# Performance work log

Measured on AMD Instinct MI355X. Metric: run time of the kernel, lower is better.

Reference implementation:

```python
import jax, jax.numpy as jnp
import numpy as np

Q_DEFAULT = 8
XI_MAX = 0.4          # center frequency of the highest-frequency wavelet (cycles/sample)
BW_RATIO = 0.8        # bandwidth-to-center-frequency ratio
LOG_EPS = 1e-6


def _make_filters(T, Q):
    """Morlet-style analytic filter bank in the Fourier domain (all static numpy)."""
    J = int(np.floor(np.log2(T / 2)))
    freqs = np.fft.fftfreq(T).astype(np.float32)          # [T], in [-0.5, 0.5)
    # first-order wavelets: J*Q filters, geometrically spaced, quality factor Q
    n1 = J * Q
    xi1 = (XI_MAX * 2.0 ** (-np.arange(n1) / Q)).astype(np.float32)
    sig1 = (BW_RATIO * xi1 / Q).astype(np.float32)
    psi1 = np.exp(-(freqs[None, :] - xi1[:, None]) ** 2 / (2.0 * sig1[:, None] ** 2)).astype(np.float32)  # [n1, T]
    # second-order wavelets: Q2 = 1, one per octave
    xi2 = (XI_MAX * 2.0 ** (-np.arange(J))).astype(np.float32)
    sig2 = (BW_RATIO * xi2).astype(np.float32)
    psi2 = np.exp(-(freqs[None, :] - xi2[:, None]) ** 2 / (2.0 * sig2[:, None] ** 2)).astype(np.float32)  # [J, T]
    # low-pass (phi): Gaussian at scale 2^J
    sigma_phi = np.float32(BW_RATIO * XI_MAX * 2.0 ** (-J))
    phi = np.exp(-(freqs ** 2) / (2.0 * sigma_phi ** 2)).astype(np.float32)  # [T]
    # valid second-order paths: xi2 strictly below xi1 (frequency-decreasing cascade)
    pair_j1, pair_k = [], []
    for k in range(J):
        for j1 in range(n1):
            if xi2[k] < xi1[j1]:
                pair_j1.append(j1)
                pair_k.append(k)
    return psi1, psi2, phi, np.asarray(pair_j1, np.int32), np.asarray(pair_k, np.int32)


def _scatter(x_flat, psi1, psi2, phi, pair_j1, pair_k):
    """x_flat: [N, T] real. Returns S: [N, 1 + n1 + n_pairs, T]."""
    xh = jnp.fft.fft(x_flat)                                   # [N, T] complex
    S0 = jnp.fft.ifft(xh * phi).real[:, None, :]               # order 0 (dropped later)
    U1 = jnp.abs(jnp.fft.ifft(xh[:, None, :] * psi1[None]))    # [N, n1, T]
    U1h = jnp.fft.fft(U1)
    S1 = jnp.fft.ifft(U1h * phi).real                          # [N, n1, T]
    U2 = jnp.abs(jnp.fft.ifft(U1h[:, pair_j1, :] * psi2[pair_k][None]))  # [N, P, T]
    S2 = jnp.fft.ifft(jnp.fft.fft(U2) * phi).real              # [N, P, T]
    return jnp.concatenate([S0, S1, S2], axis=1)


def setup_inputs() -> dict:
    key = jax.random.key(0)
    x = jax.random.normal(key, (8, 2048, 6), dtype=jnp.float32)
    return {"x": x}


def reference(x):
    B, T, C = x.shape
    psi1, psi2, phi, pj, pk = _make_filters(T, Q_DEFAULT)
    psi1, psi2, phi = jnp.asarray(psi1), jnp.asarray(psi2), jnp.asarray(phi)
    # vectorize the original per-channel Python loop: fold channels into batch
    xf = jnp.transpose(x, (0, 2, 1)).reshape(B * C, T)          # [B*C, T]
    S = _scatter(xf, psi1, psi2, phi, pj, pk)                   # [B*C, n_coef+1, T]
    out = jnp.mean(jnp.log(S[:, 1:, :] + LOG_EPS), axis=-1)     # drop order-0, log, time-mean
    return out.reshape(B, C, -1).transpose(0, 2, 1)             # [B, n_coef, C]
```

## Files before the change

kernel.cpp:

```cpp
#include <hip/hip_runtime.h>

#define NTH 256
#define U1H_STRIDE 21504

#define PHI1 0.29504296f
#define PHI2 0.0075683594f
#define GCUT 18.0f

__device__ __forceinline__ int swz(int i) { return i ^ (((i >> 4) & 3) * 5); }

__device__ __forceinline__ float2 cmul(float2 a, float2 b) {
  return make_float2(a.x * b.x - a.y * b.y, a.x * b.y + a.y * b.x);
}

template <int W>
__device__ __forceinline__ float wsum(float v) {
#pragma unroll
  for (int off = 1; off < W; off <<= 1) v += __shfl_xor(v, off, 64);
  return v;
}

__device__ __forceinline__ float2 shflx2(float2 v, int mask) {
  return make_float2(__shfl_xor(v.x, mask, 64), __shfl_xor(v.y, mask, 64));
}

template <int M, int LANES, bool INV>
__device__ __forceinline__ void rdif(float2* x, int l) {
  constexpr int R = M / LANES;
#pragma unroll
  for (int half = R / 2; half >= 1; half >>= 1) {
    const int s = half * LANES;
    const float a0 = (INV ? 3.14159265358979f : -3.14159265358979f) / (float)s;
#pragma unroll
    for (int r = 0; r < R; ++r) {
      if ((r & half) == 0) {
        const float2 a = x[r], b = x[r + half];
        const int j = (r & (half - 1)) * LANES + l;
        float2 w; __sincosf(a0 * (float)j, &w.y, &w.x);
        x[r] = make_float2(a.x + b.x, a.y + b.y);
        x[r + half] = cmul(make_float2(a.x - b.x, a.y - b.y), w);
      }
    }
  }
#pragma unroll
  for (int s = LANES / 2; s >= 1; s >>= 1) {
    const float a0 = (INV ? 3.14159265358979f : -3.14159265358979f) / (float)s;
    float2 w; __sincosf(a0 * (float)(l & (s - 1)), &w.y, &w.x);
    const bool hi = (l & s) != 0;
#pragma unroll
    for (int r = 0; r < R; ++r) {
      const float2 y = shflx2(x[r], s);
      const float2 sum = make_float2(x[r].x + y.x, x[r].y + y.y);
      const float2 dif = cmul(make_float2(y.x - x[r].x, y.y - x[r].y), w);
      x[r] = hi ? dif : sum;
    }
  }
}

template <int M, int LANES, bool INV>
__device__ __forceinline__ void rdit(float2* x, int l) {
  constexpr int R = M / LANES;
#pragma unroll
  for (int s = 1; s <= LANES / 2; s <<= 1) {
    const float a0 = (INV ? 3.14159265358979f : -3.14159265358979f) / (float)s;
    float2 w; __sincosf(a0 * (float)(l & (s - 1)), &w.y, &w.x);
    const bool hi = (l & s) != 0;
#pragma unroll
    for (int r = 0; r < R; ++r) {
      const float2 y = shflx2(x[r], s);
      const float2 wb = cmul(w, hi ? x[r] : y);
      x[r] = hi ? make_float2(y.x - wb.x, y.y - wb.y)
                : make_float2(x[r].x + wb.x, x[r].y + wb.y);
    }
  }
#pragma unroll
  for (int half = 1; half <= R / 2; half <<= 1) {
    const int s = half * LANES;
    const float a0 = (INV ? 3.14159265358979f : -3.14159265358979f) / (float)s;
#pragma unroll
    for (int r = 0; r < R; ++r) {
      if ((r & half) == 0) {
        const int j = (r & (half - 1)) * LANES + l;
        float2 w; __sincosf(a0 * (float)j, &w.y, &w.x);
        const float2 bw = cmul(x[r + half], w);
        const float2 a = x[r];
        x[r] = make_float2(a.x + bw.x, a.y + bw.y);
        x[r + half] = make_float2(a.x - bw.x, a.y - bw.y);
      }
    }
  }
}

template <bool INV>
__device__ __forceinline__ void dif4(float2* A, int j, int ls, float astep) {
  const int s = 1 << ls;
  const int e = j & (s - 1);
  const int base = ((j >> ls) << (ls + 2)) | e;
  float2 w1;
  __sincosf(astep * (float)e, &w1.y, &w1.x);
  if (INV) w1.y = -w1.y;
  const float2 w2 = cmul(w1, w1);
  const float2 w3 = cmul(w2, w1);
  const float2 a0 = A[swz(base)];
  const float2 a1 = A[swz(base + s)];
  const float2 a2 = A[swz(base + 2 * s)];
  const float2 a3 = A[swz(base + 3 * s)];
  const float t0x = a0.x + a2.x, t0y = a0.y + a2.y;
  const float t1x = a0.x - a2.x, t1y = a0.y - a2.y;
  const float t2x = a1.x + a3.x, t2y = a1.y + a3.y;
  const float bdx = a1.x - a3.x, bdy = a1.y - a3.y;
  const float sgn = INV ? -1.0f : 1.0f;
  const float t3x = sgn * bdy, t3y = -sgn * bdx;
  A[swz(base)]         = make_float2(t0x + t2x, t0y + t2y);
  A[swz(base + s)]     = cmul(make_float2(t1x + t3x, t1y + t3y), w1);
  A[swz(base + 2 * s)] = cmul(make_float2(t0x - t2x, t0y - t2y), w2);
  A[swz(base + 3 * s)] = cmul(make_float2(t1x - t3x, t1y - t3y), w3);
}

__device__ __forceinline__ void r2pair(float2* A, int g) {
  const float2 a = A[swz(2 * g)];
  const float2 b = A[swz(2 * g + 1)];
  A[swz(2 * g)]     = make_float2(a.x + b.x, a.y + b.y);
  A[swz(2 * g + 1)] = make_float2(a.x - b.x, a.y - b.y);
}

__device__ __forceinline__ int prev2048(int i) {
  return ((i >> 9) & 3) | (((i >> 7) & 3) << 2) | (((i >> 5) & 3) << 4) |
         (((i >> 3) & 3) << 6) | (((i >> 1) & 3) << 8) | ((i & 1) << 10);
}

__global__ __launch_bounds__(NTH) void kA(const float* __restrict__ x,
                                          float2* __restrict__ xh) {
  __shared__ float2 A[2048];
  const int n = blockIdx.x, b = n / 6, c = n % 6;
  const float* xp = x + (size_t)b * (2048 * 6) + c;
#pragma unroll
  for (int i = 0; i < 8; ++i) {
    const int t = (int)threadIdx.x + NTH * i;
    A[swz(t)] = make_float2(xp[t * 6], 0.0f);
  }
  const int tid = (int)threadIdx.x;
#pragma unroll
  for (int ls = 9; ls >= 1; ls -= 2) {
    const float astep = -1.5707963267948966f / (float)(1 << ls);
    __syncthreads();
#pragma unroll
    for (int i = 0; i < 2; ++i) dif4<false>(A, tid + NTH * i, ls, astep);
  }
  __syncthreads();
#pragma unroll
  for (int i = 0; i < 4; ++i) r2pair(A, tid + NTH * i);
  __syncthreads();
#pragma unroll
  for (int i = 0; i < 8; ++i) {
    const int t = (int)threadIdx.x + NTH * i;
    xh[(size_t)n * 2048 + prev2048(t)] = A[swz(t)];
  }
}

__device__ __forceinline__ int u1h_off(int j1) {
  const int o = j1 >> 3;
  if (o == 0) return j1 * 1024;
  if (o == 1) return 8192 + (j1 - 8) * 512;
  if (o == 2) return 12288 + (j1 - 16) * 256;
  return 14336 + (j1 - 24) * 128;
}
__device__ __forceinline__ float* o1p(float* out, int b, int c, int j1) {
  return out + ((size_t)b * 440 + j1) * 6 + c;
}
__device__ __forceinline__ float* o2p(float* out, int b, int c, int j1, int k) {
  return out + ((size_t)b * 440 + 80 + 4 * k * (k - 1) + j1) * 6 + c;
}
__device__ __forceinline__ float xi2f(int k) { return 0.4f * exp2f(-(float)k); }

template <int M1, int LANES>
__device__ __forceinline__ void parentR(const float2* __restrict__ src,
                                        float2* __restrict__ Vg,
                                        float* __restrict__ outp,
                                        int j1, int lane) {
  constexpr int R = M1 / LANES;
  constexpr int F = 2048 / M1;
  const int l = lane & (LANES - 1);
  const int gb = lane - l;
  const float xi = 0.4f * exp2f(-0.125f * (float)j1);
  const float sig = 0.1f * xi;
  const float i2s = 1.0f / (2.0f * sig * sig);
  float2 x[R];
#pragma unroll
  for (int r = 0; r < R; ++r) {
    const int m = r * LANES + l;
    float2 acc = make_float2(0.0f, 0.0f);
#pragma unroll
    for (int q = 0; q < F; ++q) {
      const int f = m + q * M1;
      const float fr = (float)(f < 1024 ? f : f - 2048) * (1.0f / 2048.0f);
      const float d = fr - xi;
      const float dd = d * d * i2s;
      if (dd < GCUT) {
        const float g = __expf(-dd);
        const float2 v = src[f];
        acc.x += v.x * g; acc.y += v.y * g;
      }
    }
    x[r] = acc;
  }
  rdif<M1, LANES, true>(x, l);
#pragma unroll
  for (int r = 0; r < R; ++r)
    x[r] = make_float2(sqrtf(x[r].x * x[r].x + x[r].y * x[r].y) * (1.0f / 2048.0f), 0.0f);
  rdit<M1, LANES, false>(x, l);
#pragma unroll
  for (int r = 0; r < R; ++r) Vg[r * LANES + l] = x[r];
  const float invM = 1.0f / (float)M1;
  const float c0 = __shfl(x[0].x, gb, 64) * invM;
  const float2 U1 = make_float2(__shfl(x[0].x, gb + 1, 64), __shfl(x[0].y, gb + 1, 64));
  const float2 U2 = make_float2(__shfl(x[0].x, gb + 2, 64), __shfl(x[0].y, gb + 2, 64));
  const float k1 = PHI1 * 2.0f * invM, k2 = PHI2 * 2.0f * invM;
  float part = 0.0f;
#pragma unroll
  for (int r = 0; r < R; ++r) {
    const int t = r * LANES + l;
    float sv, cv;
    __sincosf((6.283185307179586f / (float)M1) * (float)t, &sv, &cv);
    float acc = c0 + k1 * (U1.x * cv - U1.y * sv);
    const float c2 = cv * cv - sv * sv, s2 = 2.0f * sv * cv;
    acc += k2 * (U2.x * c2 - U2.y * s2);
    part += __logf(acc + 1e-6f);
  }
  part = wsum<LANES>(part);
  if (l == 0) *outp = part * invM;
}

__global__ __launch_bounds__(NTH, 4) void kB(const float2* __restrict__ xh,
                                             float2* __restrict__ U1h,
                                             float* __restrict__ out) {
  const int ci = (int)blockIdx.x / 48;
  const int n  = (int)blockIdx.x % 48;
  const int b = n / 6, c = n % 6;
  const float2* src = xh + (size_t)n * 2048;
  float2* Vb = U1h + (size_t)n * U1H_STRIDE;
  const int tid = (int)threadIdx.x;
  const int wid = tid >> 6, lane = tid & 63;
  const int h = lane >> 5;
  const int slot = 2 * wid + h;

  if (ci < 2) {
    const int j1 = 4 * ci + wid;
    parentR<1024, 64>(src, Vb + u1h_off(j1), o1p(out, b, c, j1), j1, lane);
  } else if (ci < 4) {
    const int j1 = 8 + 4 * (ci - 2) + wid;
    parentR<512, 64>(src, Vb + u1h_off(j1), o1p(out, b, c, j1), j1, lane);
  } else if (ci < 6) {
    const int j1 = 16 + 4 * (ci - 4) + wid;
    parentR<256, 64>(src, Vb + u1h_off(j1), o1p(out, b, c, j1), j1, lane);
  } else {
    const int j1 = 24 + 8 * (ci - 6) + slot;
    parentR<128, 32>(src, Vb + u1h_off(j1), o1p(out, b, c, j1), j1, lane);
  }
}

template <int M2, int LANES>
__device__ __forceinline__ void descR(const float2* __restrict__ Vg,
                                      float* __restrict__ outp,
                                      int M1, int F, float xi, int lane) {
  constexpr int R = M2 / LANES;
  constexpr int LM = (M2 == 1024) ? 10 : (M2 == 512) ? 9 : (M2 == 256) ? 8 : 7;
  const int l = lane & (LANES - 1);
  const float sg = 0.8f * xi;
  const float i2s = 1.0f / (2.0f * sg * sg);
  float2 x[R];
#pragma unroll
  for (int r = 0; r < R; ++r) {
    const int m = r * LANES + l;
    float2 acc = make_float2(0.0f, 0.0f);
    for (int q = 0; q < F; ++q) {
      const int f = m + q * M2;
      const float fr = (float)(f < (M1 >> 1) ? f : f - M1) * (1.0f / 2048.0f);
      const float d = fr - xi;
      const float dd = d * d * i2s;
      if (dd < GCUT) {
        const float g = __expf(-dd);
        const float2 vv = Vg[f];
        acc.x += vv.x * g; acc.y += vv.y * g;
      }
    }
    x[r] = acc;
  }
  rdif<M2, LANES, true>(x, l);
  const float invM1f = 1.0f / (float)M1;
  float b0 = 0, b1r = 0, b1i = 0, b2r = 0, b2i = 0;
#pragma unroll
  for (int r = 0; r < R; ++r) {
    const float u = sqrtf(x[r].x * x[r].x + x[r].y * x[r].y) * invM1f;
    const int e = r * LANES + l;
    const int t = (int)(__brev((unsigned)e) >> (32 - LM));
    float sv, cv;
    __sincosf((6.283185307179586f / (float)M2) * (float)t, &sv, &cv);
    b0 += u;
    b1r += u * cv; b1i -= u * sv;
    const float c2 = cv * cv - sv * sv, s2 = 2.0f * sv * cv;
    b2r += u * c2; b2i -= u * s2;
  }
  b0 = wsum<LANES>(b0);
  b1r = wsum<LANES>(b1r); b1i = wsum<LANES>(b1i);
  b2r = wsum<LANES>(b2r); b2i = wsum<LANES>(b2i);
  const float k1 = 2.0f * PHI1, k2 = 2.0f * PHI2;
  const float invM2 = 1.0f / (float)M2;
  float part = 0.0f;
#pragma unroll
  for (int r = 0; r < R; ++r) {
    const int e = r * LANES + l;
    const int t = (int)(__brev((unsigned)e) >> (32 - LM));
    float sv, cv;
    __sincosf((6.283185307179586f / (float)M2) * (float)t, &sv, &cv);
    float acc = b0 + k1 * (b1r * cv - b1i * sv);
    const float c2 = cv * cv - sv * sv, s2 = 2.0f * sv * cv;
    acc += k2 * (b2r * c2 - b2i * s2);
    part += __logf(acc * invM2 + 1e-6f);
  }
  part = wsum<LANES>(part);
  if (l == 0) *outp = part * invM2;
}

__global__ __launch_bounds__(NTH, 4) void kC(const float2* __restrict__ U1h,
                                             float* __restrict__ out) {
  const int ci = (int)blockIdx.x / 48;
  const int n  = (int)blockIdx.x % 48;
  const int b = n / 6, c = n % 6;
  const float2* Vb = U1h + (size_t)n * U1H_STRIDE;
  const int tid = (int)threadIdx.x;
  const int wid = tid >> 6, lane = tid & 63;
  const int h = lane >> 5;
  const int slot = 2 * wid + h;

  if (ci < 2) {
    const int j1 = 4 * ci + wid;
    descR<1024, 64>(Vb + u1h_off(j1), o2p(out, b, c, j1, 1), 1024, 1, xi2f(1), lane);
  } else if (ci < 6) {
    const int j1 = 4 * (ci - 2) + wid;
    const int M1 = (j1 < 8) ? 1024 : 512;
    descR<512, 64>(Vb + u1h_off(j1), o2p(out, b, c, j1, 2), M1, M1 / 512, xi2f(2), lane);
  } else if (ci < 8) {
    const int j1 = 4 * (ci - 6) + wid;
    descR<512, 64>(Vb + u1h_off(j1), o2p(out, b, c, j1, 3), 1024, 2, xi2f(3), lane);
  } else if (ci < 12) {
    const int j1 = 8 + 4 * (ci - 8) + wid;
    const int M1 = (j1 < 16) ? 512 : 256;
    descR<256, 64>(Vb + u1h_off(j1), o2p(out, b, c, j1, 3), M1, M1 / 256, xi2f(3), lane);
  } else if (ci < 14) {
    const int j1 = 4 * (ci - 12) + wid;
    descR<256, 64>(Vb + u1h_off(j1), o2p(out, b, c, j1, 4), 1024, 4, xi2f(4), lane);
  } else if (ci < 17) {
    const int j1 = 8 + 8 * (ci - 14) + slot;
    const int o = j1 >> 3;
    const int M1 = (o < 3) ? (1024 >> o) : 128;
    descR<128, 32>(Vb + u1h_off(j1), o2p(out, b, c, j1, 4), M1, M1 / 128, xi2f(4), lane);
  } else {
    int g = ci - 17;
    int k = 5;
    while (g >= k) { g -= k; ++k; }
    const int j1 = 8 * g + slot;
    const int M1 = (g < 3) ? (1024 >> g) : 128;
    descR<128, 32>(Vb + u1h_off(j1), o2p(out, b, c, j1, k), M1, M1 / 128, xi2f(k), lane);
  }
}

extern "C" void kernel_launch(void* const* d_in, const int* in_sizes, int n_in,
                              void* d_out, int out_size, void* d_ws, size_t ws_size,
                              hipStream_t stream) {
  (void)in_sizes; (void)n_in; (void)out_size; (void)ws_size;
  const float* x = (const float*)d_in[0];
  float* out = (float*)d_out;
  float2* U1h = (float2*)d_ws;
  float2* xh = (float2*)((char*)d_ws + (size_t)48 * U1H_STRIDE * sizeof(float2));
  kA<<<dim3(48), dim3(NTH), 0, stream>>>(x, xh);
  kB<<<dim3(13 * 48), dim3(NTH), 0, stream>>>(xh, U1h, out);
  kC<<<dim3(52 * 48), dim3(NTH), 0, stream>>>(U1h, out);
}
```

Before: 99.50 us.

## Fuse first- and second-order stages into one kernel with recomputed parents in LDS

Merges kernels kB and kC into a single kernel kU. Each wave or half-wave recomputes its first-order parent U1h from xh, then runs its second-order descendant on it directly in shared memory. This removes the global U1h round trip and one kernel launch. The register/shuffle radix-2 FFTs are replaced by radix-4 shared-memory FFTs. The trade-off is that each parent FFT is now redone for every descendant, and the extra shared memory may lower occupancy.

```diff
diff --git a/kernel.cpp b/kernel.cpp
--- a/kernel.cpp
+++ b/kernel.cpp
@@ -1,7 +1,6 @@
 #include <hip/hip_runtime.h>
 
 #define NTH 256
-#define U1H_STRIDE 21504
 
 #define PHI1 0.29504296f
 #define PHI2 0.0075683594f
@@ -20,75 +19,21 @@
   return v;
 }
 
-__device__ __forceinline__ float2 shflx2(float2 v, int mask) {
-  return make_float2(__shfl_xor(v.x, mask, 64), __shfl_xor(v.y, mask, 64));
-}
-
-template <int M, int LANES, bool INV>
-__device__ __forceinline__ void rdif(float2* x, int l) {
-  constexpr int R = M / LANES;
-#pragma unroll
-  for (int half = R / 2; half >= 1; half >>= 1) {
-    const int s = half * LANES;
-    const float a0 = (INV ? 3.14159265358979f : -3.14159265358979f) / (float)s;
-#pragma unroll
-    for (int r = 0; r < R; ++r) {
-      if ((r & half) == 0) {
-        const float2 a = x[r], b = x[r + half];
-        const int j = (r & (half - 1)) * LANES + l;
-        float2 w; __sincosf(a0 * (float)j, &w.y, &w.x);
-        x[r] = make_float2(a.x + b.x, a.y + b.y);
-        x[r + half] = cmul(make_float2(a.x - b.x, a.y - b.y), w);
-      }
-    }
-  }
-#pragma unroll
-  for (int s = LANES / 2; s >= 1; s >>= 1) {
-    const float a0 = (INV ? 3.14159265358979f : -3.14159265358979f) / (float)s;
-    float2 w; __sincosf(a0 * (float)(l & (s - 1)), &w.y, &w.x);
-    const bool hi = (l & s) != 0;
-#pragma unroll
-    for (int r = 0; r < R; ++r) {
-      const float2 y = shflx2(x[r], s);
-      const float2 sum = make_float2(x[r].x + y.x, x[r].y + y.y);
-      const float2 dif = cmul(make_float2(y.x - x[r].x, y.y - x[r].y), w);
-      x[r] = hi ? dif : sum;
-    }
-  }
-}
-
-template <int M, int LANES, bool INV>
-__device__ __forceinline__ void rdit(float2* x, int l) {
-  constexpr int R = M / LANES;
-#pragma unroll
-  for (int s = 1; s <= LANES / 2; s <<= 1) {
-    const float a0 = (INV ? 3.14159265358979f : -3.14159265358979f) / (float)s;
-    float2 w; __sincosf(a0 * (float)(l & (s - 1)), &w.y, &w.x);
-    const bool hi = (l & s) != 0;
-#pragma unroll
-    for (int r = 0; r < R; ++r) {
-      const float2 y = shflx2(x[r], s);
-      const float2 wb = cmul(w, hi ? x[r] : y);
-      x[r] = hi ? make_float2(y.x - wb.x, y.y - wb.y)
-                : make_float2(x[r].x + wb.x, x[r].y + wb.y);
-    }
-  }
-#pragma unroll
-  for (int half = 1; half <= R / 2; half <<= 1) {
-    const int s = half * LANES;
-    const float a0 = (INV ? 3.14159265358979f : -3.14159265358979f) / (float)s;
-#pragma unroll
-    for (int r = 0; r < R; ++r) {
-      if ((r & half) == 0) {
-        const int j = (r & (half - 1)) * LANES + l;
-        float2 w; __sincosf(a0 * (float)j, &w.y, &w.x);
-        const float2 bw = cmul(x[r + half], w);
-        const float2 a = x[r];
-        x[r] = make_float2(a.x + bw.x, a.y + bw.y);
-        x[r + half] = make_float2(a.x - bw.x, a.y - bw.y);
-      }
-    }
-  }
+template <int M>
+__device__ __forceinline__ int prevM(int i) {
+  if (M == 128)
+    return ((i >> 5) & 3) | (((i >> 3) & 3) << 2) | (((i >> 1) & 3) << 4) | ((i & 1) << 6);
+  else if (M == 256)
+    return ((i & 3) << 6) | (((i >> 2) & 3) << 4) | (((i >> 4) & 3) << 2) | ((i >> 6) & 3);
+  else if (M == 512)
+    return ((i >> 7) & 3) | (((i >> 5) & 3) << 2) | (((i >> 3) & 3) << 4) |
+           (((i >> 1) & 3) << 6) | ((i & 1) << 8);
+  else if (M == 1024)
+    return ((i >> 8) & 3) | (((i >> 6) & 3) << 2) | (((i >> 4) & 3) << 4) |
+           (((i >> 2) & 3) << 6) | ((i & 3) << 8);
+  else
+    return ((i >> 9) & 3) | (((i >> 7) & 3) << 2) | (((i >> 5) & 3) << 4) |
+           (((i >> 3) & 3) << 6) | (((i >> 1) & 3) << 8) | ((i & 1) << 10);
 }
 
 template <bool INV>
@@ -117,6 +62,29 @@
   A[swz(base + 3 * s)] = cmul(make_float2(t1x - t3x, t1y - t3y), w3);
 }
 
+__device__ __forceinline__ void dit4(float2* A, int j, int ls, float astep) {
+  const int s = 1 << ls;
+  const int e = j & (s - 1);
+  const int base = ((j >> ls) << (ls + 2)) | e;
+  float2 w1;
+  __sincosf(astep * (float)e, &w1.y, &w1.x);
+  const float2 w2 = cmul(w1, w1);
+  const float2 w3 = cmul(w2, w1);
+  const float2 c0 = A[swz(base)];
+  const float2 c1 = cmul(A[swz(base + s)], w1);
+  const float2 c2 = cmul(A[swz(base + 2 * s)], w2);
+  const float2 c3 = cmul(A[swz(base + 3 * s)], w3);
+  const float t0x = c0.x + c2.x, t0y = c0.y + c2.y;
+  const float t1x = c0.x - c2.x, t1y = c0.y - c2.y;
+  const float t2x = c1.x + c3.x, t2y = c1.y + c3.y;
+  const float bdx = c1.x - c3.x, bdy = c1.y - c3.y;
+  const float t3x = bdy, t3y = -bdx;
+  A[swz(base)]         = make_float2(t0x + t2x, t0y + t2y);
+  A[swz(base + s)]     = make_float2(t1x + t3x, t1y + t3y);
+  A[swz(base + 2 * s)] = make_float2(t0x - t2x, t0y - t2y);
+  A[swz(base + 3 * s)] = make_float2(t1x - t3x, t1y - t3y);
+}
+
 __device__ __forceinline__ void r2pair(float2* A, int g) {
   const float2 a = A[swz(2 * g)];
   const float2 b = A[swz(2 * g + 1)];
@@ -124,6 +92,41 @@
   A[swz(2 * g + 1)] = make_float2(a.x - b.x, a.y - b.y);
 }
 
+template <int M> struct LMof { static constexpr int v =
+  (M == 2048) ? 11 : (M == 1024) ? 10 : (M == 512) ? 9 : (M == 256) ? 8 : 7; };
+
+template <int M, bool INV, int LANES>
+__device__ __forceinline__ void dif_w(float2* Aw, int l) {
+  constexpr int LM = LMof<M>::v;
+  constexpr int NB = M / 4;
+#pragma unroll
+  for (int ls = LM - 2; ls >= (LM & 1); ls -= 2) {
+    const float astep = -1.5707963267948966f / (float)(1 << ls);
+#pragma unroll
+    for (int i = 0; i < NB / LANES; ++i) dif4<INV>(Aw, l + LANES * i, ls, astep);
+  }
+  if (LM & 1) {
+#pragma unroll
+    for (int i = 0; i < (M / 2) / LANES; ++i) r2pair(Aw, l + LANES * i);
+  }
+}
+
+template <int M, int LANES>
+__device__ __forceinline__ void dit_w(float2* Aw, int l) {
+  constexpr int LM = LMof<M>::v;
+  constexpr int NB = M / 4;
+  if (LM & 1) {
+#pragma unroll
+    for (int i = 0; i < (M / 2) / LANES; ++i) r2pair(Aw, l + LANES * i);
+  }
+#pragma unroll
+  for (int ls = (LM & 1); ls <= LM - 2; ls += 2) {
+    const float astep = -1.5707963267948966f / (float)(1 << ls);
+#pragma unroll
+    for (int i = 0; i < NB / LANES; ++i) dit4(Aw, l + LANES * i, ls, astep);
+  }
+}
+
 __device__ __forceinline__ int prev2048(int i) {
   return ((i >> 9) & 3) | (((i >> 7) & 3) << 2) | (((i >> 5) & 3) << 4) |
          (((i >> 3) & 3) << 6) | (((i >> 1) & 3) << 8) | ((i & 1) << 10);
@@ -158,13 +161,6 @@
   }
 }
 
-__device__ __forceinline__ int u1h_off(int j1) {
-  const int o = j1 >> 3;
-  if (o == 0) return j1 * 1024;
-  if (o == 1) return 8192 + (j1 - 8) * 512;
-  if (o == 2) return 12288 + (j1 - 16) * 256;
-  return 14336 + (j1 - 24) * 128;
-}
 __device__ __forceinline__ float* o1p(float* out, int b, int c, int j1) {
   return out + ((size_t)b * 440 + j1) * 6 + c;
 }
@@ -174,21 +170,16 @@
 __device__ __forceinline__ float xi2f(int k) { return 0.4f * exp2f(-(float)k); }
 
 template <int M1, int LANES>
-__device__ __forceinline__ void parentR(const float2* __restrict__ src,
-                                        float2* __restrict__ Vg,
-                                        float* __restrict__ outp,
-                                        int j1, int lane) {
-  constexpr int R = M1 / LANES;
+__device__ __forceinline__ void parent_w(float2* Vw, const float2* __restrict__ src,
+                                         float* s1p, int j1, int l) {
+  constexpr int NRW = M1 / LANES;
   constexpr int F = 2048 / M1;
-  const int l = lane & (LANES - 1);
-  const int gb = lane - l;
   const float xi = 0.4f * exp2f(-0.125f * (float)j1);
   const float sig = 0.1f * xi;
   const float i2s = 1.0f / (2.0f * sig * sig);
-  float2 x[R];
-#pragma unroll
-  for (int r = 0; r < R; ++r) {
-    const int m = r * LANES + l;
+#pragma unroll
+  for (int i = 0; i < NRW; ++i) {
+    const int m = l + LANES * i;
     float2 acc = make_float2(0.0f, 0.0f);
 #pragma unroll
     for (int q = 0; q < F; ++q) {
@@ -202,75 +193,45 @@
         acc.x += v.x * g; acc.y += v.y * g;
       }
     }
-    x[r] = acc;
-  }
-  rdif<M1, LANES, true>(x, l);
-#pragma unroll
-  for (int r = 0; r < R; ++r)
-    x[r] = make_float2(sqrtf(x[r].x * x[r].x + x[r].y * x[r].y) * (1.0f / 2048.0f), 0.0f);
-  rdit<M1, LANES, false>(x, l);
-#pragma unroll
-  for (int r = 0; r < R; ++r) Vg[r * LANES + l] = x[r];
-  const float invM = 1.0f / (float)M1;
-  const float c0 = __shfl(x[0].x, gb, 64) * invM;
-  const float2 U1 = make_float2(__shfl(x[0].x, gb + 1, 64), __shfl(x[0].y, gb + 1, 64));
-  const float2 U2 = make_float2(__shfl(x[0].x, gb + 2, 64), __shfl(x[0].y, gb + 2, 64));
-  const float k1 = PHI1 * 2.0f * invM, k2 = PHI2 * 2.0f * invM;
-  float part = 0.0f;
-#pragma unroll
-  for (int r = 0; r < R; ++r) {
-    const int t = r * LANES + l;
-    float sv, cv;
-    __sincosf((6.283185307179586f / (float)M1) * (float)t, &sv, &cv);
-    float acc = c0 + k1 * (U1.x * cv - U1.y * sv);
-    const float c2 = cv * cv - sv * sv, s2 = 2.0f * sv * cv;
-    acc += k2 * (U2.x * c2 - U2.y * s2);
-    part += __logf(acc + 1e-6f);
-  }
-  part = wsum<LANES>(part);
-  if (l == 0) *outp = part * invM;
-}
-
-__global__ __launch_bounds__(NTH, 4) void kB(const float2* __restrict__ xh,
-                                             float2* __restrict__ U1h,
-                                             float* __restrict__ out) {
-  const int ci = (int)blockIdx.x / 48;
-  const int n  = (int)blockIdx.x % 48;
-  const int b = n / 6, c = n % 6;
-  const float2* src = xh + (size_t)n * 2048;
-  float2* Vb = U1h + (size_t)n * U1H_STRIDE;
-  const int tid = (int)threadIdx.x;
-  const int wid = tid >> 6, lane = tid & 63;
-  const int h = lane >> 5;
-  const int slot = 2 * wid + h;
-
-  if (ci < 2) {
-    const int j1 = 4 * ci + wid;
-    parentR<1024, 64>(src, Vb + u1h_off(j1), o1p(out, b, c, j1), j1, lane);
-  } else if (ci < 4) {
-    const int j1 = 8 + 4 * (ci - 2) + wid;
-    parentR<512, 64>(src, Vb + u1h_off(j1), o1p(out, b, c, j1), j1, lane);
-  } else if (ci < 6) {
-    const int j1 = 16 + 4 * (ci - 4) + wid;
-    parentR<256, 64>(src, Vb + u1h_off(j1), o1p(out, b, c, j1), j1, lane);
-  } else {
-    const int j1 = 24 + 8 * (ci - 6) + slot;
-    parentR<128, 32>(src, Vb + u1h_off(j1), o1p(out, b, c, j1), j1, lane);
+    Vw[swz(m)] = acc;
+  }
+  dif_w<M1, true, LANES>(Vw, l);
+#pragma unroll
+  for (int i = 0; i < NRW; ++i) {
+    const int m = l + LANES * i;
+    const float2 zv = Vw[swz(m)];
+    Vw[swz(m)] = make_float2(sqrtf(zv.x * zv.x + zv.y * zv.y) * (1.0f / 2048.0f), 0.0f);
+  }
+  dit_w<M1, LANES>(Vw, l);
+  if (s1p) {
+    const float invM = 1.0f / (float)M1;
+    const float c0 = Vw[0].x * invM;
+    const float2 U1 = Vw[1], U2 = Vw[2];
+    const float k1 = PHI1 * 2.0f * invM, k2 = PHI2 * 2.0f * invM;
+    float part = 0.0f;
+#pragma unroll
+    for (int i = 0; i < NRW; ++i) {
+      const int t = l + LANES * i;
+      float sv, cv;
+      __sincosf((6.283185307179586f / (float)M1) * (float)t, &sv, &cv);
+      float acc = c0 + k1 * (U1.x * cv - U1.y * sv);
+      const float c2 = cv * cv - sv * sv, s2 = 2.0f * sv * cv;
+      acc += k2 * (U2.x * c2 - U2.y * s2);
+      part += __logf(acc + 1e-6f);
+    }
+    part = wsum<LANES>(part);
+    if (l == 0) *s1p = part * invM;
   }
 }
 
 template <int M2, int LANES>
-__device__ __forceinline__ void descR(const float2* __restrict__ Vg,
-                                      float* __restrict__ outp,
-                                      int M1, int F, float xi, int lane) {
-  constexpr int R = M2 / LANES;
-  constexpr int LM = (M2 == 1024) ? 10 : (M2 == 512) ? 9 : (M2 == 256) ? 8 : 7;
-  const int l = lane & (LANES - 1);
+__device__ __forceinline__ void desc_ip(float2* Vw, float* __restrict__ outp,
+                                        int M1, int F, float xi, int l) {
+  constexpr int NR2 = M2 / LANES;
   const float sg = 0.8f * xi;
   const float i2s = 1.0f / (2.0f * sg * sg);
-  float2 x[R];
-#pragma unroll
-  for (int r = 0; r < R; ++r) {
+#pragma unroll
+  for (int r = 0; r < NR2; ++r) {
     const int m = r * LANES + l;
     float2 acc = make_float2(0.0f, 0.0f);
     for (int q = 0; q < F; ++q) {
@@ -280,20 +241,21 @@
       const float dd = d * d * i2s;
       if (dd < GCUT) {
         const float g = __expf(-dd);
-        const float2 vv = Vg[f];
+        const float2 vv = Vw[swz(f)];
         acc.x += vv.x * g; acc.y += vv.y * g;
       }
     }
-    x[r] = acc;
-  }
-  rdif<M2, LANES, true>(x, l);
+    Vw[swz(m)] = acc;
+  }
+  dif_w<M2, true, LANES>(Vw, l);
   const float invM1f = 1.0f / (float)M1;
   float b0 = 0, b1r = 0, b1i = 0, b2r = 0, b2i = 0;
 #pragma unroll
-  for (int r = 0; r < R; ++r) {
-    const float u = sqrtf(x[r].x * x[r].x + x[r].y * x[r].y) * invM1f;
-    const int e = r * LANES + l;
-    const int t = (int)(__brev((unsigned)e) >> (32 - LM));
+  for (int r = 0; r < NR2; ++r) {
+    const int idx = r * LANES + l;
+    const float2 zv = Vw[swz(idx)];
+    const float u = sqrtf(zv.x * zv.x + zv.y * zv.y) * invM1f;
+    const int t = prevM<M2>(idx);
     float sv, cv;
     __sincosf((6.283185307179586f / (float)M2) * (float)t, &sv, &cv);
     b0 += u;
@@ -308,9 +270,9 @@
   const float invM2 = 1.0f / (float)M2;
   float part = 0.0f;
 #pragma unroll
-  for (int r = 0; r < R; ++r) {
-    const int e = r * LANES + l;
-    const int t = (int)(__brev((unsigned)e) >> (32 - LM));
+  for (int r = 0; r < NR2; ++r) {
+    const int idx = r * LANES + l;
+    const int t = prevM<M2>(idx);
     float sv, cv;
     __sincosf((6.283185307179586f / (float)M2) * (float)t, &sv, &cv);
     float acc = b0 + k1 * (b1r * cv - b1i * sv);
@@ -322,46 +284,66 @@
   if (l == 0) *outp = part * invM2;
 }
 
-__global__ __launch_bounds__(NTH, 4) void kC(const float2* __restrict__ U1h,
+__global__ __launch_bounds__(NTH, 4) void kU(const float2* __restrict__ xh,
                                              float* __restrict__ out) {
+  __shared__ float2 L[4096];
   const int ci = (int)blockIdx.x / 48;
   const int n  = (int)blockIdx.x % 48;
   const int b = n / 6, c = n % 6;
-  const float2* Vb = U1h + (size_t)n * U1H_STRIDE;
+  const float2* src = xh + (size_t)n * 2048;
   const int tid = (int)threadIdx.x;
-  const int wid = tid >> 6, lane = tid & 63;
-  const int h = lane >> 5;
+  const int wid = tid >> 6, l = tid & 63;
+  const int h = l >> 5, ll = l & 31;
   const int slot = 2 * wid + h;
 
-  if (ci < 2) {
-    const int j1 = 4 * ci + wid;
-    descR<1024, 64>(Vb + u1h_off(j1), o2p(out, b, c, j1, 1), 1024, 1, xi2f(1), lane);
-  } else if (ci < 6) {
-    const int j1 = 4 * (ci - 2) + wid;
-    const int M1 = (j1 < 8) ? 1024 : 512;
-    descR<512, 64>(Vb + u1h_off(j1), o2p(out, b, c, j1, 2), M1, M1 / 512, xi2f(2), lane);
-  } else if (ci < 8) {
-    const int j1 = 4 * (ci - 6) + wid;
-    descR<512, 64>(Vb + u1h_off(j1), o2p(out, b, c, j1, 3), 1024, 2, xi2f(3), lane);
-  } else if (ci < 12) {
-    const int j1 = 8 + 4 * (ci - 8) + wid;
-    const int M1 = (j1 < 16) ? 512 : 256;
-    descR<256, 64>(Vb + u1h_off(j1), o2p(out, b, c, j1, 3), M1, M1 / 256, xi2f(3), lane);
-  } else if (ci < 14) {
-    const int j1 = 4 * (ci - 12) + wid;
-    descR<256, 64>(Vb + u1h_off(j1), o2p(out, b, c, j1, 4), 1024, 4, xi2f(4), lane);
-  } else if (ci < 17) {
-    const int j1 = 8 + 8 * (ci - 14) + slot;
-    const int o = j1 >> 3;
-    const int M1 = (o < 3) ? (1024 >> o) : 128;
-    descR<128, 32>(Vb + u1h_off(j1), o2p(out, b, c, j1, 4), M1, M1 / 128, xi2f(4), lane);
+  if (ci < 48) {
+    const int ft = ci * 4 + wid;
+    int j1, k, M1;
+    bool s1;
+    if (ft < 72) {
+      j1 = ft / 9; k = 1 + ft % 9; M1 = 1024; s1 = (ft % 9 == 0);
+    } else if (ft < 136) {
+      const int t = ft - 72;
+      j1 = 8 + (t >> 3); k = 2 + (t & 7); M1 = 512; s1 = ((t & 7) == 0);
+    } else {
+      const int t = ft - 136;
+      j1 = 16 + t / 7; k = 3 + t % 7; M1 = 256; s1 = (t % 7 == 0);
+    }
+    float2* Vw = L + wid * 1024;
+    float* s1ptr = s1 ? o1p(out, b, c, j1) : nullptr;
+    if (M1 == 1024)      parent_w<1024, 64>(Vw, src, s1ptr, j1, l);
+    else if (M1 == 512)  parent_w<512, 64>(Vw, src, s1ptr, j1, l);
+    else                 parent_w<256, 64>(Vw, src, s1ptr, j1, l);
+    const float xk = xi2f(k);
+    float* op = o2p(out, b, c, j1, k);
+    if (k == 1) {
+      desc_ip<1024, 64>(Vw, op, 1024, 1, xk, l);
+    } else if (k == 2) {
+      desc_ip<512, 64>(Vw, op, M1, M1 >> 9, xk, l);
+    } else if (k == 3) {
+      if (M1 == 1024) desc_ip<512, 64>(Vw, op, 1024, 2, xk, l);
+      else            desc_ip<256, 64>(Vw, op, M1, M1 >> 8, xk, l);
+    } else if (k == 4 && M1 == 1024) {
+      desc_ip<256, 64>(Vw, op, 1024, 4, xk, l);
+    } else {
+      if (h == 0) desc_ip<128, 32>(Vw, op, M1, M1 >> 7, xk, ll);
+    }
   } else {
-    int g = ci - 17;
-    int k = 5;
-    while (g >= k) { g -= k; ++k; }
-    const int j1 = 8 * g + slot;
-    const int M1 = (g < 3) ? (1024 >> g) : 128;
-    descR<128, 32>(Vb + u1h_off(j1), o2p(out, b, c, j1, k), M1, M1 / 128, xi2f(k), lane);
+    const int ht = (ci - 48) * 8 + slot;
+    int j1, k = 0;
+    bool s1, havedesc = true;
+    if (ht < 48)       { const int t = ht;       j1 = 24 + t / 6; k = 4 + t % 6; s1 = (t % 6 == 0); }
+    else if (ht < 88)  { const int t = ht - 48;  j1 = 32 + t / 5; k = 5 + t % 5; s1 = (t % 5 == 0); }
+    else if (ht < 120) { const int t = ht - 88;  j1 = 40 + (t >> 2); k = 6 + (t & 3); s1 = ((t & 3) == 0); }
+    else if (ht < 144) { const int t = ht - 120; j1 = 48 + t / 3; k = 7 + t % 3; s1 = (t % 3 == 0); }
+    else if (ht < 160) { const int t = ht - 144; j1 = 56 + (t >> 1); k = 8 + (t & 1); s1 = ((t & 1) == 0); }
+    else if (ht < 168) { j1 = 64 + (ht - 160); k = 9; s1 = true; }
+    else               { j1 = 72 + (ht - 168); s1 = true; havedesc = false; }
+    float2* Vh = L + slot * 128;
+    float* s1ptr = s1 ? o1p(out, b, c, j1) : nullptr;
+    parent_w<128, 32>(Vh, src, s1ptr, j1, ll);
+    if (havedesc)
+      desc_ip<128, 32>(Vh, o2p(out, b, c, j1, k), 128, 1, xi2f(k), ll);
   }
 }
 
@@ -371,9 +353,7 @@
   (void)in_sizes; (void)n_in; (void)out_size; (void)ws_size;
   const float* x = (const float*)d_in[0];
   float* out = (float*)d_out;
-  float2* U1h = (float2*)d_ws;
-  float2* xh = (float2*)((char*)d_ws + (size_t)48 * U1H_STRIDE * sizeof(float2));
+  float2* xh = (float2*)d_ws;
   kA<<<dim3(48), dim3(NTH), 0, stream>>>(x, xh);
-  kB<<<dim3(13 * 48), dim3(NTH), 0, stream>>>(xh, U1h, out);
-  kC<<<dim3(52 * 48), dim3(NTH), 0, stream>>>(U1h, out);
-}
+  kU<<<dim3(70 * 48), dim3(NTH), 0, stream>>>(xh, out);
+}
```

Measured after the change: 148.6 us. 1.49x slower.
